# Kernel optimization log

Hardware: AMD Instinct MI355X
Metric: run time of the kernel (lower is better)

Reference implementation:

```python
import jax, jax.numpy as jnp
import numpy as np

DIM = 128
B, N = 2, 72


def setup_inputs() -> dict:
    key = jax.random.key(0)
    ks = jax.random.split(key, 6)
    s = 1.0 / np.sqrt(DIM)
    s3 = 1.0 / np.sqrt(3 * DIM)
    return {
        "node_emb": jax.random.normal(ks[0], (B * N, DIM), dtype=jnp.float32),
        "path_emb": jax.random.normal(ks[1], (B, N, N, DIM), dtype=jnp.float32),
        "W_hz": jax.random.uniform(ks[2], (DIM, DIM), minval=-s, maxval=s, dtype=jnp.float32),
        "b_hz": jax.random.uniform(ks[3], (DIM,), minval=-s, maxval=s, dtype=jnp.float32),
        "W_zz": jax.random.uniform(ks[4], (3 * DIM, DIM), minval=-s3, maxval=s3, dtype=jnp.float32),
        "b_zz": jax.random.uniform(ks[5], (DIM,), minval=-s3, maxval=s3, dtype=jnp.float32),
    }


def reference(node_emb, path_emb, W_hz, b_hz, W_zz, b_zz):
    b, n, _, d = path_emb.shape
    # z = W_hz(path_emb)
    z = jnp.einsum('bijd,de->bije', path_emb, W_hz) + b_hz
    # tropical (max-plus) triangle aggregation: out[b,i,j,d] = max_k z[b,i,k,d] + z[b,k,j,d]
    z_conv = jnp.max(z[:, :, :, None, :] + z[:, None, :, :, :], axis=2)  # (b,n,n,d)
    # path_aggr with mode 'max' -> elementwise max of z_conv and z
    z = jnp.maximum(z_conv, z)
    ne = node_emb.reshape(b, n, d)
    n_i = jnp.broadcast_to(ne[:, :, None, :], (b, n, n, d))
    n_j = jnp.broadcast_to(ne[:, None, :, :], (b, n, n, d))
    zc = jnp.concatenate([n_i, z, n_j], axis=-1)  # (b,n,n,3d)
    out = jax.nn.relu(jnp.einsum('bijc,ce->bije', zc, W_zz) + b_zz)
    return out
```

## Files before the change

### kernel.cpp

```cpp
#include <hip/hip_runtime.h>

#define DIM 128
#define NN 72
#define BB 2
#define NSQ (NN*NN)
#define NROWS (BB*NSQ)
#define BN (BB*NN)
#define ZBLOCKS (NROWS/16)

__global__ __launch_bounds__(256, 4) void k_phase1(const float* __restrict__ path,
                                                   const float* __restrict__ Whz,
                                                   const float* __restrict__ bhz,
                                                   float* __restrict__ z,
                                                   float* __restrict__ zT,
                                                   const float* __restrict__ node,
                                                   const float* __restrict__ Wzz,
                                                   float* __restrict__ P1,
                                                   float* __restrict__ P3) {
    __shared__ float rows[16 * DIM];
    const int t = threadIdx.x;

    if (blockIdx.x < ZBLOCKS) {
        const int r0 = blockIdx.x * 16;
        {
            float4* rs = (float4*)rows;
            const float4* pg = (const float4*)(path + r0 * DIM);
            rs[t]       = pg[t];
            rs[t + 256] = pg[t + 256];
        }
        __syncthreads();

        const int e2 = t & 63;
        const int rg = t >> 6;
        float2 bz = *(const float2*)&bhz[2 * e2];
        float2 acc[4];
#pragma unroll
        for (int r = 0; r < 4; r++) acc[r] = bz;

        const float* Wp = Whz + 2 * e2;
        float2 w0[4], w1[4], n0[4], n1[4];
#pragma unroll
        for (int dd = 0; dd < 4; dd++) {
            w0[dd] = *(const float2*)&Wp[dd * DIM];
            w1[dd] = *(const float2*)&Wp[(4 + dd) * DIM];
        }
        for (int d8 = 0; d8 < 16; d8++) {
            if (d8 < 15) {
#pragma unroll
                for (int dd = 0; dd < 4; dd++) {
                    n0[dd] = *(const float2*)&Wp[(8 * d8 + 8 + dd) * DIM];
                    n1[dd] = *(const float2*)&Wp[(8 * d8 + 12 + dd) * DIM];
                }
            }
            float4 pa[4], pb[4];
#pragma unroll
            for (int r = 0; r < 4; r++) {
                pa[r] = *(const float4*)&rows[(rg + 4 * r) * DIM + 8 * d8];
                pb[r] = *(const float4*)&rows[(rg + 4 * r) * DIM + 8 * d8 + 4];
            }
#pragma unroll
            for (int dd = 0; dd < 4; dd++)
#pragma unroll
                for (int r = 0; r < 4; r++) {
                    float pv = ((const float*)&pa[r])[dd];
                    acc[r].x = fmaf(pv, w0[dd].x, acc[r].x);
                    acc[r].y = fmaf(pv, w0[dd].y, acc[r].y);
                }
#pragma unroll
            for (int dd = 0; dd < 4; dd++)
#pragma unroll
                for (int r = 0; r < 4; r++) {
                    float pv = ((const float*)&pb[r])[dd];
                    acc[r].x = fmaf(pv, w1[dd].x, acc[r].x);
                    acc[r].y = fmaf(pv, w1[dd].y, acc[r].y);
                }
#pragma unroll
            for (int dd = 0; dd < 4; dd++) { w0[dd] = n0[dd]; w1[dd] = n1[dd]; }
        }
#pragma unroll
        for (int r = 0; r < 4; r++) {
            int row = r0 + rg + 4 * r;
            *(float2*)&z[row * DIM + 2 * e2] = acc[r];
            int b  = row / NSQ;
            int ij = row - b * NSQ;
            int i  = ij / NN;
            int j  = ij - i * NN;
            *(float2*)&zT[(b * NSQ + j * NN + i) * DIM + 2 * e2] = acc[r];
        }
    } else {
        const int r0 = (blockIdx.x - ZBLOCKS) * 8;
        {
            float4* rs = (float4*)rows;
            const float4* ng = (const float4*)(node + r0 * DIM);
            rs[t] = ng[t];
        }
        __syncthreads();
        const int e  = t & 127;
        const int rr = t >> 7;
        float a1[4] = {0.f, 0.f, 0.f, 0.f};
        float a3[4] = {0.f, 0.f, 0.f, 0.f};
        const float* W1 = Wzz + e;
        const float* W3 = Wzz + 2 * DIM * DIM + e;
        for (int d = 0; d < DIM; d++) {
            float w1 = W1[d * DIM];
            float w3 = W3[d * DIM];
#pragma unroll
            for (int s = 0; s < 4; s++) {
                float pv = rows[(rr + 2 * s) * DIM + d];
                a1[s] = fmaf(pv, w1, a1[s]);
                a3[s] = fmaf(pv, w3, a3[s]);
            }
        }
#pragma unroll
        for (int s = 0; s < 4; s++) {
            int m = r0 + rr + 2 * s;
            P1[m * DIM + e] = a1[s];
            P3[m * DIM + e] = a3[s];
        }
    }
}

__global__ __launch_bounds__(256, 3) void k_trop_out(
        const float* __restrict__ z,   const float* __restrict__ zT,
        const float* __restrict__ Wzz, const float* __restrict__ bzz,
        const float* __restrict__ P1,  const float* __restrict__ P3,
        float* __restrict__ out) {
    __shared__ float rows[16 * DIM];
    __shared__ float comb[16 * DIM];
    const int t   = threadIdx.x;
    const int blk = blockIdx.x;
    const int xcd  = blk & 7;
    const int slot = blk >> 3;
    const int b  = xcd >> 2;
    const int qi = (xcd >> 1) & 1;
    const int qj = xcd & 1;
    const int il = slot / 9;
    const int jl = slot - il * 9;
    const int it = qi * 9 + il;
    const int jt = qj * 9 + jl;
    const int i0 = it * 4, j0 = jt * 4;
    const int d  = t & 127;
    const int ty = t >> 7;
    const float* zb  = z  + b * NSQ * DIM;
    const float* zTb = zT + b * NSQ * DIM;

    {
        float acc[16];
#pragma unroll
        for (int q = 0; q < 16; q++) acc[q] = -3.402823466e38f;

        float cur[32], nxt[32];
#pragma unroll
        for (int kk = 0; kk < 4; kk++) {
            int k = ty + 2 * kk;
#pragma unroll
            for (int s = 0; s < 4; s++) {
                cur[kk * 8 + s]     = zb [((i0 + s) * NN + k) * DIM + d];
                cur[kk * 8 + 4 + s] = zTb[((j0 + s) * NN + k) * DIM + d];
            }
        }
        for (int g = 0; g < 9; g++) {
            if (g < 8) {
#pragma unroll
                for (int kk = 0; kk < 4; kk++) {
                    int k = ty + 2 * kk + 8 * (g + 1);
#pragma unroll
                    for (int s = 0; s < 4; s++) {
                        nxt[kk * 8 + s]     = zb [((i0 + s) * NN + k) * DIM + d];
                        nxt[kk * 8 + 4 + s] = zTb[((j0 + s) * NN + k) * DIM + d];
                    }
                }
            }
#pragma unroll
            for (int kk = 0; kk < 4; kk++)
#pragma unroll
                for (int a = 0; a < 4; a++)
#pragma unroll
                    for (int c = 0; c < 4; c++)
                        acc[a * 4 + c] = fmaxf(acc[a * 4 + c],
                                               cur[kk * 8 + a] + cur[kk * 8 + 4 + c]);
#pragma unroll
            for (int q = 0; q < 32; q++) cur[q] = nxt[q];
        }

        if (ty == 1) {
#pragma unroll
            for (int q = 0; q < 16; q++) comb[q * DIM + d] = acc[q];
        }
        __syncthreads();
        if (ty == 0) {
#pragma unroll
            for (int a = 0; a < 4; a++)
#pragma unroll
                for (int c = 0; c < 4; c++) {
                    int q = a * 4 + c;
                    float m = fmaxf(acc[q], comb[q * DIM + d]);
                    int idx = ((i0 + a) * NN + (j0 + c)) * DIM + d;
                    rows[q * DIM + d] = fmaxf(m, zb[idx]);
                }
        }
    }
    __syncthreads();

    {
        const int e2 = t & 63;
        const int rg = t >> 6;
        float2 acc[4];
#pragma unroll
        for (int r = 0; r < 4; r++) acc[r] = make_float2(0.f, 0.f);

        const float* Wp = Wzz + DIM * DIM + 2 * e2;
        float2 w0[4], w1[4], n0[4], n1[4];
#pragma unroll
        for (int dd = 0; dd < 4; dd++) {
            w0[dd] = *(const float2*)&Wp[dd * DIM];
            w1[dd] = *(const float2*)&Wp[(4 + dd) * DIM];
        }
        for (int d8 = 0; d8 < 16; d8++) {
            if (d8 < 15) {
#pragma unroll
                for (int dd = 0; dd < 4; dd++) {
                    n0[dd] = *(const float2*)&Wp[(8 * d8 + 8 + dd) * DIM];
                    n1[dd] = *(const float2*)&Wp[(8 * d8 + 12 + dd) * DIM];
                }
            }
            float4 pa[4], pb[4];
#pragma unroll
            for (int r = 0; r < 4; r++) {
                pa[r] = *(const float4*)&rows[(rg + 4 * r) * DIM + 8 * d8];
                pb[r] = *(const float4*)&rows[(rg + 4 * r) * DIM + 8 * d8 + 4];
            }
#pragma unroll
            for (int dd = 0; dd < 4; dd++)
#pragma unroll
                for (int r = 0; r < 4; r++) {
                    float pv = ((const float*)&pa[r])[dd];
                    acc[r].x = fmaf(pv, w0[dd].x, acc[r].x);
                    acc[r].y = fmaf(pv, w0[dd].y, acc[r].y);
                }
#pragma unroll
            for (int dd = 0; dd < 4; dd++)
#pragma unroll
                for (int r = 0; r < 4; r++) {
                    float pv = ((const float*)&pb[r])[dd];
                    acc[r].x = fmaf(pv, w1[dd].x, acc[r].x);
                    acc[r].y = fmaf(pv, w1[dd].y, acc[r].y);
                }
#pragma unroll
            for (int dd = 0; dd < 4; dd++) { w0[dd] = n0[dd]; w1[dd] = n1[dd]; }
        }

        float2 bz = *(const float2*)&bzz[2 * e2];
#pragma unroll
        for (int r = 0; r < 4; r++) {
            int q = rg + 4 * r;
            int a = q >> 2, c = q & 3;
            int orow = b * NSQ + (i0 + a) * NN + (j0 + c);
            float2 v1 = *(const float2*)&P1[(b * NN + i0 + a) * DIM + 2 * e2];
            float2 v3 = *(const float2*)&P3[(b * NN + j0 + c) * DIM + 2 * e2];
            float ox = fmaxf(acc[r].x + v1.x + v3.x + bz.x, 0.f);
            float oy = fmaxf(acc[r].y + v1.y + v3.y + bz.y, 0.f);
            *(float2*)&out[orow * DIM + 2 * e2] = make_float2(ox, oy);
        }
    }
}

extern "C" void kernel_launch(void* const* d_in, const int* in_sizes, int n_in,
                              void* d_out, int out_size, void* d_ws, size_t ws_size,
                              hipStream_t stream) {
    const float* node = (const float*)d_in[0];
    const float* path = (const float*)d_in[1];
    const float* Whz  = (const float*)d_in[2];
    const float* bhz  = (const float*)d_in[3];
    const float* Wzz  = (const float*)d_in[4];
    const float* bzz  = (const float*)d_in[5];
    float* out = (float*)d_out;

    float* z  = (float*)d_ws;
    float* zT = z  + NROWS * DIM;
    float* P1 = zT + NROWS * DIM;
    float* P3 = P1 + BN * DIM;

    hipLaunchKernelGGL(k_phase1,   dim3(ZBLOCKS + 18), dim3(256), 0, stream,
                       path, Whz, bhz, z, zT, node, Wzz, P1, P3);
    hipLaunchKernelGGL(k_trop_out, dim3(BB * 18 * 18), dim3(256), 0, stream,
                       z, zT, Wzz, bzz, P1, P3, out);
}
```

Before: 107.3 us.

## Drop transposed z copy and split tropical k-range across four thread groups

Stops writing the transposed zT buffer in phase 1 and reads z[k,j] directly in the tropical kernel, which removes a scattered global write of the whole z tensor. The tropical loop now has each thread handle two channels with float2 loads, and splits k into four contiguous ranges of 18 across four 64-thread groups. Partial maxima are combined through shared memory in a two-level reduction with extra barriers. Memory traffic in phase 1 drops, while the tropical kernel takes more synchronization and different access strides.

```diff
diff --git a/kernel.cpp b/kernel.cpp
--- a/kernel.cpp
+++ b/kernel.cpp
@@ -12,7 +12,6 @@
                                                    const float* __restrict__ Whz,
                                                    const float* __restrict__ bhz,
                                                    float* __restrict__ z,
-                                                   float* __restrict__ zT,
                                                    const float* __restrict__ node,
                                                    const float* __restrict__ Wzz,
                                                    float* __restrict__ P1,
@@ -81,11 +80,6 @@
         for (int r = 0; r < 4; r++) {
             int row = r0 + rg + 4 * r;
             *(float2*)&z[row * DIM + 2 * e2] = acc[r];
-            int b  = row / NSQ;
-            int ij = row - b * NSQ;
-            int i  = ij / NN;
-            int j  = ij - i * NN;
-            *(float2*)&zT[(b * NSQ + j * NN + i) * DIM + 2 * e2] = acc[r];
         }
     } else {
         const int r0 = (blockIdx.x - ZBLOCKS) * 8;
@@ -121,7 +115,7 @@
 }
 
 __global__ __launch_bounds__(256, 3) void k_trop_out(
-        const float* __restrict__ z,   const float* __restrict__ zT,
+        const float* __restrict__ z,
         const float* __restrict__ Wzz, const float* __restrict__ bzz,
         const float* __restrict__ P1,  const float* __restrict__ P3,
         float* __restrict__ out) {
@@ -139,53 +133,84 @@
     const int it = qi * 9 + il;
     const int jt = qj * 9 + jl;
     const int i0 = it * 4, j0 = jt * 4;
-    const int d  = t & 127;
-    const int ty = t >> 7;
-    const float* zb  = z  + b * NSQ * DIM;
-    const float* zTb = zT + b * NSQ * DIM;
+    const int e  = t & 63;
+    const int ty = t >> 6;
+    const float* zb = z + b * NSQ * DIM;
 
     {
-        float acc[16];
-#pragma unroll
-        for (int q = 0; q < 16; q++) acc[q] = -3.402823466e38f;
-
-        float cur[32], nxt[32];
-#pragma unroll
-        for (int kk = 0; kk < 4; kk++) {
-            int k = ty + 2 * kk;
+        float2 acc[16];
+#pragma unroll
+        for (int q = 0; q < 16; q++)
+            acc[q] = make_float2(-3.402823466e38f, -3.402823466e38f);
+
+        const int kbase = 18 * ty;
+        float2 cur[16], nxt[16];
+#pragma unroll
+        for (int kk = 0; kk < 2; kk++) {
+            int k = kbase + kk;
 #pragma unroll
             for (int s = 0; s < 4; s++) {
-                cur[kk * 8 + s]     = zb [((i0 + s) * NN + k) * DIM + d];
-                cur[kk * 8 + 4 + s] = zTb[((j0 + s) * NN + k) * DIM + d];
+                cur[kk * 8 + s]     = *(const float2*)&zb[((i0 + s) * NN + k) * DIM + 2 * e];
+                cur[kk * 8 + 4 + s] = *(const float2*)&zb[(k * NN + (j0 + s)) * DIM + 2 * e];
             }
         }
         for (int g = 0; g < 9; g++) {
             if (g < 8) {
 #pragma unroll
-                for (int kk = 0; kk < 4; kk++) {
-                    int k = ty + 2 * kk + 8 * (g + 1);
+                for (int kk = 0; kk < 2; kk++) {
+                    int k = kbase + 2 * (g + 1) + kk;
 #pragma unroll
                     for (int s = 0; s < 4; s++) {
-                        nxt[kk * 8 + s]     = zb [((i0 + s) * NN + k) * DIM + d];
-                        nxt[kk * 8 + 4 + s] = zTb[((j0 + s) * NN + k) * DIM + d];
+                        nxt[kk * 8 + s]     = *(const float2*)&zb[((i0 + s) * NN + k) * DIM + 2 * e];
+                        nxt[kk * 8 + 4 + s] = *(const float2*)&zb[(k * NN + (j0 + s)) * DIM + 2 * e];
                     }
                 }
             }
 #pragma unroll
-            for (int kk = 0; kk < 4; kk++)
+            for (int kk = 0; kk < 2; kk++)
 #pragma unroll
                 for (int a = 0; a < 4; a++)
 #pragma unroll
-                    for (int c = 0; c < 4; c++)
-                        acc[a * 4 + c] = fmaxf(acc[a * 4 + c],
-                                               cur[kk * 8 + a] + cur[kk * 8 + 4 + c]);
-#pragma unroll
-            for (int q = 0; q < 32; q++) cur[q] = nxt[q];
-        }
-
+                    for (int c = 0; c < 4; c++) {
+                        int q = a * 4 + c;
+                        float sx = cur[kk * 8 + a].x + cur[kk * 8 + 4 + c].x;
+                        float sy = cur[kk * 8 + a].y + cur[kk * 8 + 4 + c].y;
+                        acc[q].x = fmaxf(acc[q].x, sx);
+                        acc[q].y = fmaxf(acc[q].y, sy);
+                    }
+#pragma unroll
+            for (int q = 0; q < 16; q++) cur[q] = nxt[q];
+        }
+
+        if (ty == 2) {
+#pragma unroll
+            for (int q = 0; q < 16; q++) *(float2*)&comb[q * DIM + 2 * e] = acc[q];
+        }
+        if (ty == 3) {
+#pragma unroll
+            for (int q = 0; q < 16; q++) *(float2*)&rows[q * DIM + 2 * e] = acc[q];
+        }
+        __syncthreads();
+        if (ty == 0) {
+#pragma unroll
+            for (int q = 0; q < 16; q++) {
+                float2 v = *(const float2*)&comb[q * DIM + 2 * e];
+                acc[q].x = fmaxf(acc[q].x, v.x);
+                acc[q].y = fmaxf(acc[q].y, v.y);
+            }
+        }
         if (ty == 1) {
 #pragma unroll
-            for (int q = 0; q < 16; q++) comb[q * DIM + d] = acc[q];
+            for (int q = 0; q < 16; q++) {
+                float2 v = *(const float2*)&rows[q * DIM + 2 * e];
+                acc[q].x = fmaxf(acc[q].x, v.x);
+                acc[q].y = fmaxf(acc[q].y, v.y);
+            }
+        }
+        __syncthreads();
+        if (ty == 1) {
+#pragma unroll
+            for (int q = 0; q < 16; q++) *(float2*)&comb[q * DIM + 2 * e] = acc[q];
         }
         __syncthreads();
         if (ty == 0) {
@@ -194,9 +219,11 @@
 #pragma unroll
                 for (int c = 0; c < 4; c++) {
                     int q = a * 4 + c;
-                    float m = fmaxf(acc[q], comb[q * DIM + d]);
-                    int idx = ((i0 + a) * NN + (j0 + c)) * DIM + d;
-                    rows[q * DIM + d] = fmaxf(m, zb[idx]);
+                    float2 v  = *(const float2*)&comb[q * DIM + 2 * e];
+                    float2 zd = *(const float2*)&zb[((i0 + a) * NN + (j0 + c)) * DIM + 2 * e];
+                    float mx = fmaxf(fmaxf(acc[q].x, v.x), zd.x);
+                    float my = fmaxf(fmaxf(acc[q].y, v.y), zd.y);
+                    *(float2*)&rows[q * DIM + 2 * e] = make_float2(mx, my);
                 }
         }
     }
@@ -277,12 +304,11 @@
     float* out = (float*)d_out;
 
     float* z  = (float*)d_ws;
-    float* zT = z  + NROWS * DIM;
-    float* P1 = zT + NROWS * DIM;
+    float* P1 = z  + NROWS * DIM;
     float* P3 = P1 + BN * DIM;
 
     hipLaunchKernelGGL(k_phase1,   dim3(ZBLOCKS + 18), dim3(256), 0, stream,
-                       path, Whz, bhz, z, zT, node, Wzz, P1, P3);
+                       path, Whz, bhz, z, node, Wzz, P1, P3);
     hipLaunchKernelGGL(k_trop_out, dim3(BB * 18 * 18), dim3(256), 0, stream,
-                       z, zT, Wzz, bzz, P1, P3, out);
+                       z, Wzz, bzz, P1, P3, out);
 }
```

After: 109.1 us. About the same (+1.6%).
